# Optimization experiments

Measured on AMD Instinct MI355X. Metric: run time of the kernel, lower is better.

The kernel has to match this reference:

```python
import jax, jax.numpy as jnp
import numpy as np

DIM = 128  # parameter size fixed in __init__


def _rope_rows(x, c):
    """Apply rope_flash to the [c, DIM] matrix formed by repeating x (shape [DIM]) c times.
    axis=0 -> position = arange(c); half_size = DIM // 2."""
    half = DIM // 2
    pos = jnp.arange(c, dtype=jnp.float32)  # [c]
    inv_freq = 10000.0 ** (-(jnp.arange(half, dtype=jnp.float32) / float(half)))  # [half]
    sinusoid = pos[:, None] * inv_freq[None, :]  # [c, half]
    sin = jnp.sin(sinusoid)
    cos = jnp.cos(sinusoid)
    x1 = x[:half]  # [half], constant across rows (row-repeat of the param)
    x2 = x[half:]
    # broadcast [half] against [c, half]
    return jnp.concatenate([x1 * cos - x2 * sin, x2 * cos + x1 * sin], axis=-1)  # [c, DIM]


def setup_inputs() -> dict:
    key = jax.random.key(0)
    ka, kb = jax.random.split(key)
    # truncated_normal_(std=0.02) init approximated with scaled normals (values irrelevant to math)
    a = jax.random.normal(ka, (DIM,), dtype=jnp.float32) * 0.02
    b = jax.random.normal(kb, (DIM,), dtype=jnp.float32) * 0.02
    return {"a": a, "b": b, "c": 8192}


def reference(a, b, c):
    a_rot = _rope_rows(a, c)  # [c, DIM]
    b_rot = _rope_rows(b, c)  # [c, DIM]
    # einsum('mk,nk->mn')
    return jnp.einsum('mk,nk->mn', a_rot, b_rot)  # [c, c]
```

## Files before the change

### kernel.cpp

```cpp
#include <hip/hip_runtime.h>


#define CSEQ 8192
#define HALF 64
#define GOFF (CSEQ - 1)

__global__ __launch_bounds__(256) void compute_g_kernel(
    const float* __restrict__ a, const float* __restrict__ b,
    float* __restrict__ g) {
    int d = blockIdx.x * blockDim.x + threadIdx.x;
    if (d >= CSEQ) return;
    float sP = 0.0f;
    float sQ = 0.0f;
    const float df = (float)d;
    #pragma unroll 8
    for (int j = 0; j < HALF; ++j) {
        float a1 = a[j], a2 = a[j + HALF];
        float b1 = b[j], b2 = b[j + HALF];
        float P = a1 * b1 + a2 * b2;
        float Q = a1 * b2 - a2 * b1;
        float f = exp2f(-0.20762050593046014f * (float)j);
        float s, c;
        sincosf(df * f, &s, &c);
        sP = fmaf(P, c, sP);
        sQ = fmaf(Q, s, sQ);
    }
    g[GOFF + d] = sP + sQ;
    g[GOFF - d] = sP - sQ;
}

__global__ __launch_bounds__(256) void fill_out_kernel(
    const float* __restrict__ g, float* __restrict__ out) {
    unsigned tid = blockIdx.x * blockDim.x + threadIdx.x;
    unsigned m  = tid >> 11;
    unsigned n0 = (tid & 2047u) << 2;
    const float* gp = g + (int)(GOFF + m - n0);
    float4 v;
    v.x = gp[0];
    v.y = gp[-1];
    v.z = gp[-2];
    v.w = gp[-3];
    *reinterpret_cast<float4*>(out + (size_t)m * CSEQ + n0) = v;
}

extern "C" void kernel_launch(void* const* d_in, const int* in_sizes, int n_in,
                              void* d_out, int out_size, void* d_ws, size_t ws_size,
                              hipStream_t stream) {
    const float* a = (const float*)d_in[0];
    const float* b = (const float*)d_in[1];
    float* g   = (float*)d_ws;
    float* out = (float*)d_out;

    compute_g_kernel<<<CSEQ / 256, 256, 0, stream>>>(a, b, g);

    const unsigned total4 = (CSEQ * CSEQ) / 4;
    fill_out_kernel<<<total4 / 256, 256, 0, stream>>>(g, out);
}
```

Baseline: 261.3 us.

## Parallelize g computation across wavefront lanes and stage Toeplitz fill through LDS

The g-vector kernel now gives each wavefront one diagonal offset, with one lane per frequency and a shuffle reduction, instead of a serial 64-iteration loop per thread. This raises parallelism from 32 blocks to 2048. The fill kernel now loads a contiguous 1024-element window of g coalesced into shared memory in reversed order, then writes float4 rows from LDS. This replaces four misaligned, descending scalar global loads per thread. The cost is a block barrier and extra LDS traffic in the store-bound fill kernel.

```diff
diff --git a/kernel.cpp b/kernel.cpp
--- a/kernel.cpp
+++ b/kernel.cpp
@@ -8,39 +8,50 @@
 __global__ __launch_bounds__(256) void compute_g_kernel(
     const float* __restrict__ a, const float* __restrict__ b,
     float* __restrict__ g) {
-    int d = blockIdx.x * blockDim.x + threadIdx.x;
-    if (d >= CSEQ) return;
-    float sP = 0.0f;
-    float sQ = 0.0f;
-    const float df = (float)d;
-    #pragma unroll 8
-    for (int j = 0; j < HALF; ++j) {
-        float a1 = a[j], a2 = a[j + HALF];
-        float b1 = b[j], b2 = b[j + HALF];
-        float P = a1 * b1 + a2 * b2;
-        float Q = a1 * b2 - a2 * b1;
-        float f = exp2f(-0.20762050593046014f * (float)j);
-        float s, c;
-        sincosf(df * f, &s, &c);
-        sP = fmaf(P, c, sP);
-        sQ = fmaf(Q, s, sQ);
+    const int lane = threadIdx.x & 63;
+    const int d    = blockIdx.x * 4 + (threadIdx.x >> 6);
+    const int j    = lane;
+
+    float a1 = a[j], a2 = a[j + HALF];
+    float b1 = b[j], b2 = b[j + HALF];
+    float P = a1 * b1 + a2 * b2;
+    float Q = a1 * b2 - a2 * b1;
+    float f = exp2f(-0.20762050593046014f * (float)j);
+    float s, c;
+    sincosf((float)d * f, &s, &c);
+    float sP = P * c;
+    float sQ = Q * s;
+
+    #pragma unroll
+    for (int off = 32; off > 0; off >>= 1) {
+        sP += __shfl_down(sP, off, 64);
+        sQ += __shfl_down(sQ, off, 64);
     }
-    g[GOFF + d] = sP + sQ;
-    g[GOFF - d] = sP - sQ;
+    if (lane == 0) {
+        g[GOFF + d] = sP + sQ;
+        g[GOFF - d] = sP - sQ;
+    }
 }
 
 __global__ __launch_bounds__(256) void fill_out_kernel(
     const float* __restrict__ g, float* __restrict__ out) {
-    unsigned tid = blockIdx.x * blockDim.x + threadIdx.x;
-    unsigned m  = tid >> 11;
-    unsigned n0 = (tid & 2047u) << 2;
-    const float* gp = g + (int)(GOFF + m - n0);
-    float4 v;
-    v.x = gp[0];
-    v.y = gp[-1];
-    v.z = gp[-2];
-    v.w = gp[-3];
-    *reinterpret_cast<float4*>(out + (size_t)m * CSEQ + n0) = v;
+    __shared__ float lds[1024];
+    const unsigned b  = blockIdx.x;
+    const unsigned m  = b >> 3;
+    const unsigned N0 = (b & 7u) << 10;
+    const unsigned t  = threadIdx.x;
+
+    const int lo = (int)(GOFF + m) - (int)N0 - 1023;
+    #pragma unroll
+    for (int r = 0; r < 4; ++r) {
+        int j = r * 256 + (int)t;
+        lds[1023 - j] = g[lo + j];
+    }
+    __syncthreads();
+
+    const unsigned c0 = t << 2;
+    float4 v = *reinterpret_cast<const float4*>(&lds[c0]);
+    *reinterpret_cast<float4*>(out + (size_t)m * CSEQ + N0 + c0) = v;
 }
 
 extern "C" void kernel_launch(void* const* d_in, const int* in_sizes, int n_in,
@@ -51,8 +62,7 @@
     float* g   = (float*)d_ws;
     float* out = (float*)d_out;
 
-    compute_g_kernel<<<CSEQ / 256, 256, 0, stream>>>(a, b, g);
+    compute_g_kernel<<<CSEQ / 4 / 1, 256, 0, stream>>>(a, b, g);
 
-    const unsigned total4 = (CSEQ * CSEQ) / 4;
-    fill_out_kernel<<<total4 / 256, 256, 0, stream>>>(g, out);
+    fill_out_kernel<<<CSEQ * 8, 256, 0, stream>>>(g, out);
 }
```

Measured after the change: 254.0 us. -2.8%, faster.
